# Optimization experiments

Hardware: AMD Instinct MI355X
Metric: run time of the kernel (lower is better)

The kernel has to match this reference:

```python
import jax, jax.numpy as jnp
import numpy as np


def setup_inputs() -> dict:
    key = jax.random.key(0)
    ks = jax.random.split(key, 11)
    B, S, D, H, E, NS = 4, 2048, 1024, 1024, 7, 1
    sc = 0.03125  # ~1/sqrt(D) to keep activations sane
    return {
        "x": jax.random.normal(ks[0], (B, S, D), jnp.float32),
        "gate_w": jax.random.normal(ks[1], (D, E), jnp.float32) * sc,
        "gate_b": jax.random.normal(ks[2], (E,), jnp.float32) * sc,
        "biases": jnp.zeros((E,), jnp.float32),
        "w1": jax.random.normal(ks[3], (E, D, H), jnp.float32) * sc,
        "wg": jax.random.normal(ks[4], (E, D, H), jnp.float32) * sc,
        "w2": jax.random.normal(ks[5], (E, H, D), jnp.float32) * sc,
        "sw1": jax.random.normal(ks[6], (NS, D, H), jnp.float32) * sc,
        "sb1": jax.random.normal(ks[7], (NS, H), jnp.float32) * sc,
        "sw2": jax.random.normal(ks[8], (NS, H, D), jnp.float32) * sc,
        "sb2": jax.random.normal(ks[9], (NS, D), jnp.float32) * sc,
        "top_k": 3,
    }


def reference(x, gate_w, gate_b, biases, w1, wg, w2, sw1, sb1, sw2, sb2, top_k):
    B, S, D = x.shape
    E = w1.shape[0]
    N = B * S
    x2 = x.reshape(N, D)

    # Shared experts: lin1 -> silu -> lin2 (no gate branch), summed over shared dim
    h = jax.nn.silu(jnp.einsum("nd,edh->enh", x2, sw1) + sb1[:, None, :])
    shared = jnp.sum(jnp.einsum("enh,ehd->end", h, sw2) + sb2[:, None, :], axis=0)

    # Router: softmax probs, top-k on bias-adjusted probs, renormalize gathered probs
    probs = jax.nn.softmax(x2 @ gate_w + gate_b, axis=-1)  # [N, E]
    _, topk_idx = jax.lax.top_k(probs + biases, top_k)      # [N, k]
    tp = jnp.take_along_axis(probs, topk_idx, axis=-1)
    tp = tp / jnp.sum(tp, axis=-1, keepdims=True)

    # Combine weights: zero for unselected experts -> [N, E]
    combine = jnp.zeros((N, E), x2.dtype).at[jnp.arange(N)[:, None], topk_idx].add(tp)

    # Routed experts: SwiGLU FFN per expert, weighted combine
    h1 = jax.nn.silu(jnp.einsum("nd,edh->enh", x2, w1)) * jnp.einsum("nd,edh->enh", x2, wg)
    routed = jnp.einsum("enh,ehd,ne->nd", h1, w2, combine)

    return (shared + routed).reshape(B, S, D)
```

## Files before the change

### kernel.cpp

```cpp
#include <hip/hip_runtime.h>
#include <hip/hip_bf16.h>

#define N_TOK 8192
#define DIM   1024
#define NE    7
#define MT_TILES 136

typedef __attribute__((ext_vector_type(8))) short bf16x8;
typedef __attribute__((ext_vector_type(4))) float f32x4;

typedef __attribute__((address_space(3))) ushort lds_us_t;
typedef __attribute__((address_space(1))) const ushort glb_us_t;

__device__ __forceinline__ void gll16(const ushort* g, ushort* l) {
    __builtin_amdgcn_global_load_lds((glb_us_t*)g, (lds_us_t*)l, 16, 0, 0);
}

__device__ __forceinline__ unsigned short f2bf(float f) {
    unsigned int u = __builtin_bit_cast(unsigned int, f);
    u += 0x7fffu + ((u >> 16) & 1u);
    return (unsigned short)(u >> 16);
}

__device__ __forceinline__ float bf2f(unsigned short b) {
    unsigned int u = ((unsigned int)b) << 16;
    return __builtin_bit_cast(float, u);
}

__device__ __forceinline__ float siluf(float v) { return v / (1.f + __expf(-v)); }

__global__ void __launch_bounds__(256)
prep_kernel(const float* __restrict__ w1, const float* __restrict__ wg,
            const float* __restrict__ w2, const float* __restrict__ sw1,
            const float* __restrict__ sw2,
            ushort* __restrict__ w1T, ushort* __restrict__ wgT,
            ushort* __restrict__ w2T,
            const float* __restrict__ x, const float* __restrict__ gw,
            const float* __restrict__ gb, const float* __restrict__ bia,
            int* __restrict__ topk_e, float* __restrict__ topk_w,
            int* __restrict__ counts, ushort* __restrict__ xb)
{
    __shared__ float smem[NE * DIM + 8];
    const int tid = threadIdx.x;
    const int z = blockIdx.z;

    if (z < 23) {
        const float* src; ushort* dst;
        if (z < 7)       { src = w1 + (size_t)z * (DIM*DIM);        dst = w1T + (size_t)z * (DIM*DIM); }
        else if (z < 14) { src = wg + (size_t)(z - 7) * (DIM*DIM);  dst = wgT + (size_t)(z - 7) * (DIM*DIM); }
        else if (z < 21) { src = w2 + (size_t)(z - 14) * (DIM*DIM); dst = w2T + (size_t)(z - 14) * (DIM*DIM); }
        else if (z == 21){ src = sw1; dst = w1T + (size_t)NE * (DIM*DIM); }
        else             { src = sw2; dst = w2T + (size_t)NE * (DIM*DIM); }
        float (*t)[33] = (float(*)[33])smem;
        int bx = blockIdx.x * 32, by = blockIdx.y * 32;
        int lx = tid & 31, ly = tid >> 5;
#pragma unroll
        for (int i = 0; i < 32; i += 8)
            t[ly + i][lx] = src[(size_t)(by + ly + i) * DIM + bx + lx];
        __syncthreads();
#pragma unroll
        for (int i = 0; i < 32; i += 8) {
            int r = ly + i;
            dst[(size_t)(bx + r) * DIM + by + lx] = f2bf(t[lx][r]);
        }
        return;
    }

    float (*gwT)[DIM] = (float(*)[DIM])smem;
    int* cnt = (int*)(smem + NE * DIM);
    const int gblk = blockIdx.y * 32 + blockIdx.x;
    if (tid < NE) cnt[tid] = 0;
    for (int t = tid; t < NE * DIM; t += 256) {
        int d = t / NE, e = t - d * NE;
        gwT[e][d] = gw[t];
    }
    __syncthreads();

    const int lane = tid & 63, wid = tid >> 6;
#pragma unroll
    for (int tt = 0; tt < 2; tt++) {
        const int n = gblk * 8 + wid * 2 + tt;
        const float4* xr = (const float4*)(x + (size_t)n * DIM);
        ushort4* xo = (ushort4*)(xb + (size_t)n * DIM);
        float p[NE];
#pragma unroll
        for (int e = 0; e < NE; e++) p[e] = 0.f;
#pragma unroll
        for (int it = 0; it < 4; it++) {
            int i4 = it * 64 + lane;
            float4 v = xr[i4];
            ushort4 o;
            o.x = f2bf(v.x); o.y = f2bf(v.y); o.z = f2bf(v.z); o.w = f2bf(v.w);
            xo[i4] = o;
            int d = i4 * 4;
#pragma unroll
            for (int e = 0; e < NE; e++) {
                float4 g = *(const float4*)&gwT[e][d];
                p[e] += v.x * g.x + v.y * g.y + v.z * g.z + v.w * g.w;
            }
        }
#pragma unroll
        for (int e = 0; e < NE; e++)
            for (int off = 32; off; off >>= 1) p[e] += __shfl_xor(p[e], off);
        if (lane == 0) {
            float l[NE], m = -1e30f;
#pragma unroll
            for (int e = 0; e < NE; e++) { l[e] = p[e] + gb[e]; m = fmaxf(m, l[e]); }
            float s = 0.f;
#pragma unroll
            for (int e = 0; e < NE; e++) { l[e] = __expf(l[e] - m); s += l[e]; }
            float inv = 1.f / s;
#pragma unroll
            for (int e = 0; e < NE; e++) l[e] *= inv;
            float adj[NE]; bool used[NE];
#pragma unroll
            for (int e = 0; e < NE; e++) { adj[e] = l[e] + bia[e]; used[e] = false; }
            int sel[3]; float w[3]; float ws = 0.f;
            for (int k = 0; k < 3; k++) {
                int b = -1; float bv = -1e30f;
                for (int e = 0; e < NE; e++)
                    if (!used[e] && adj[e] > bv) { bv = adj[e]; b = e; }
                used[b] = true; sel[k] = b; w[k] = l[b]; ws += w[k];
            }
            float iws = 1.f / ws;
            for (int k = 0; k < 3; k++) {
                topk_e[n * 3 + k] = sel[k];
                topk_w[n * 3 + k] = w[k] * iws;
                atomicAdd(&cnt[sel[k]], 1);
            }
        }
    }
    __syncthreads();
    if (tid < NE) atomicAdd(&counts[tid], cnt[tid]);
}

__global__ void __launch_bounds__(64)
setup_kernel(int* __restrict__ ctrl)
{
    __shared__ int eoff[NE + 1];
    __shared__ int tb[NE + 1];
    const int tid = threadIdx.x;
    if (tid == 0) {
        int off = 0, t = 0;
        for (int e = 0; e < NE; e++) {
            eoff[e] = off;
            tb[e] = t;
            ctrl[16 + e] = off;
            int padc = (ctrl[8 + e] + 255) & ~255;
            off += padc;
            t += padc >> 8;
        }
        eoff[NE] = off;  tb[NE] = t;
        ctrl[2] = off;
        ctrl[1] = off + N_TOK;
        ctrl[0] = t + (N_TOK >> 8);
    }
    __syncthreads();
    if (tid <= NE) {
        int* tiles = ctrl + 32;
        int o = eoff[tid];
        int t0 = tb[tid];
        int nt = (tid == NE) ? (N_TOK >> 8) : (tb[tid + 1] - tb[tid]);
        for (int i = 0; i < nt; i++) {
            tiles[(t0 + i) * 2]     = tid;
            tiles[(t0 + i) * 2 + 1] = o + i * 256;
        }
    }
}

__global__ void __launch_bounds__(256)
scatter_kernel(const int* __restrict__ topk_e, int* __restrict__ ctrl,
               int* __restrict__ row_tok, int* __restrict__ slots)
{
    __shared__ int lcnt[NE];
    __shared__ int base[NE];
    const int tid = threadIdx.x;
    const int n = blockIdx.x * 256 + tid;
    if (tid < NE) lcnt[tid] = 0;
    __syncthreads();
    row_tok[ctrl[2] + n] = n;
    int e[3], ofs[3];
#pragma unroll
    for (int k = 0; k < 3; k++) {
        e[k] = topk_e[n * 3 + k];
        ofs[k] = atomicAdd(&lcnt[e[k]], 1);
    }
    __syncthreads();
    if (tid < NE) base[tid] = atomicAdd(&ctrl[16 + tid], lcnt[tid]);
    __syncthreads();
#pragma unroll
    for (int k = 0; k < 3; k++) {
        int slot = base[e[k]] + ofs[k];
        row_tok[slot] = n;
        slots[n * 3 + k] = slot;
    }
}


__global__ void __launch_bounds__(512, 2)
g1_kernel(const ushort* __restrict__ Xb, const ushort* __restrict__ W1,
          const ushort* __restrict__ WG, const float* __restrict__ sb1,
          ushort* __restrict__ H, const int* __restrict__ row_tok,
          const int* __restrict__ ctrl)
{
    __shared__ ushort lds[32768];
    int bx, col0;
    {
        int L = blockIdx.x + blockIdx.y * MT_TILES;
        int D = (L & 7) * MT_TILES + (L >> 3);
        bx = D >> 3;  col0 = (D & 7) * 128;
    }
    if (bx >= ctrl[0]) return;
    const int e     = ctrl[32 + 2*bx];
    const int slot0 = ctrl[32 + 2*bx + 1];
    const bool gated = (e != NE);
    const int tt = threadIdx.x;
    const int lane = tt & 63, wid = tt >> 6;
    const int wm = wid >> 1, wn = wid & 1;
    const int wofs = wid * 512;

    const int slog = (tt & 7) ^ ((tt >> 3) & 7);
    const int kk0 = (slog & 3) * 8;
    const int r0 = ((tt >> 3) << 1) + (slog >> 2);
    const ushort* pA0 = Xb + (size_t)row_tok[slot0 + r0] * DIM + kk0;
    const ushort* pA1 = Xb + (size_t)row_tok[slot0 + r0 + 128] * DIM + kk0;
    const ushort* B1e = W1 + (size_t)e * (DIM*DIM);
    const ushort* B2e = gated ? (WG + (size_t)e * (DIM*DIM))
                              : (W1 + (size_t)NE * (DIM*DIM));
    const ushort* pB1 = B1e + (size_t)(col0 + r0) * DIM + kk0;
    const ushort* pB2 = B2e + (size_t)(col0 + r0) * DIM + kk0;

    const int hi = lane >> 4, lr = lane & 15;
    int aoff[4], boff[4];
#pragma unroll
    for (int m = 0; m < 4; m++) {
        int row = wm*64 + m*16 + lr;
        int lrow = row >> 1;
        int sl = ((row & 1) << 2) | hi;
        aoff[m] = lrow*64 + (sl ^ (lrow & 7))*8;
    }
#pragma unroll
    for (int n = 0; n < 4; n++) {
        int oc = wn*64 + n*16 + lr;
        int lrow = oc >> 1;
        int sl = ((oc & 1) << 2) | hi;
        boff[n] = lrow*64 + (sl ^ (lrow & 7))*8;
    }

    f32x4 zero4 = {0.f, 0.f, 0.f, 0.f};
    f32x4 acc1[4][4], acc2[4][4];
#pragma unroll
    for (int m = 0; m < 4; m++)
#pragma unroll
        for (int n = 0; n < 4; n++) { acc1[m][n] = zero4; acc2[m][n] = zero4; }

    auto stage = [&](int buf, int kte) {
        ushort* b = &lds[buf * 16384];
        gll16(pA0 + kte, b + wofs);
        gll16(pA1 + kte, b + 4096 + wofs);
        gll16(pB1 + kte, b + 8192 + wofs);
        if (gated) gll16(pB2 + kte, b + 12288 + wofs);
    };
    auto compute = [&](int buf) {
        const ushort* Ab = &lds[buf * 16384];
        const ushort* Bb = Ab + 8192;
        bf16x8 a[4], bv[4];
#pragma unroll
        for (int m = 0; m < 4; m++) a[m] = *(const bf16x8*)(Ab + aoff[m]);
#pragma unroll
        for (int n = 0; n < 4; n++) bv[n] = *(const bf16x8*)(Bb + boff[n]);
        __builtin_amdgcn_s_setprio(1);
#pragma unroll
        for (int m = 0; m < 4; m++)
#pragma unroll
            for (int n = 0; n < 4; n++)
                acc1[m][n] = __builtin_amdgcn_mfma_f32_16x16x32_bf16(a[m], bv[n], acc1[m][n], 0, 0, 0);
        __builtin_amdgcn_s_setprio(0);
        if (gated) {
            const ushort* B2b = Ab + 12288;
            bf16x8 b2[4];
#pragma unroll
            for (int n = 0; n < 4; n++) b2[n] = *(const bf16x8*)(B2b + boff[n]);
            __builtin_amdgcn_s_setprio(1);
#pragma unroll
            for (int m = 0; m < 4; m++)
#pragma unroll
                for (int n = 0; n < 4; n++)
                    acc2[m][n] = __builtin_amdgcn_mfma_f32_16x16x32_bf16(a[m], b2[n], acc2[m][n], 0, 0, 0);
            __builtin_amdgcn_s_setprio(0);
        }
    };

    stage(0, 0);
    asm volatile("s_waitcnt vmcnt(0)" ::: "memory");
    __builtin_amdgcn_s_barrier();
    asm volatile("" ::: "memory");
    for (int t = 0; t < 31; ++t) {
        stage((t + 1) & 1, (t + 1) * 32);
        compute(t & 1);
        asm volatile("s_waitcnt vmcnt(0)" ::: "memory");
        __builtin_amdgcn_s_barrier();
        asm volatile("" ::: "memory");
    }
    compute(1);

#pragma unroll
    for (int m = 0; m < 4; m++)
#pragma unroll
        for (int n = 0; n < 4; n++)
#pragma unroll
            for (int r = 0; r < 4; r++) {
                int row = slot0 + wm*64 + m*16 + hi*4 + r;
                int col = col0 + wn*64 + n*16 + lr;
                float v1 = acc1[m][n][r];
                float h = gated ? siluf(v1) * acc2[m][n][r]
                                : siluf(v1 + sb1[col]);
                H[(size_t)row * DIM + col] = f2bf(h);
            }
}

__global__ void __launch_bounds__(512, 2)
g2_kernel(const ushort* __restrict__ H, const ushort* __restrict__ W2,
          const float* __restrict__ sb2, float* __restrict__ out,
          ushort* __restrict__ y2, const int* __restrict__ ctrl)
{
    __shared__ ushort lds[24576];
    int bx, col0;
    {
        int L = blockIdx.x + blockIdx.y * MT_TILES;
        int D = (L & 7) * MT_TILES + (L >> 3);
        bx = D >> 3;  col0 = (D & 7) * 128;
    }
    if (bx >= ctrl[0]) return;
    const int e     = ctrl[32 + 2*bx];
    const int slot0 = ctrl[32 + 2*bx + 1];
    const int sbase = ctrl[2];
    const int tt = threadIdx.x;
    const int lane = tt & 63, wid = tt >> 6;
    const int wm = wid >> 1, wn = wid & 1;
    const int wofs = wid * 512;

    const int slog = (tt & 7) ^ ((tt >> 3) & 7);
    const int kk0 = (slog & 3) * 8;
    const int r0 = ((tt >> 3) << 1) + (slog >> 2);
    const ushort* pA0 = H + (size_t)(slot0 + r0) * DIM + kk0;
    const ushort* pA1 = H + (size_t)(slot0 + r0 + 128) * DIM + kk0;
    const ushort* Be  = W2 + (size_t)e * (DIM*DIM);
    const ushort* pB1 = Be + (size_t)(col0 + r0) * DIM + kk0;

    const int hi = lane >> 4, lr = lane & 15;
    int aoff[4], boff[4];
#pragma unroll
    for (int m = 0; m < 4; m++) {
        int row = wm*64 + m*16 + lr;
        int lrow = row >> 1;
        int sl = ((row & 1) << 2) | hi;
        aoff[m] = lrow*64 + (sl ^ (lrow & 7))*8;
    }
#pragma unroll
    for (int n = 0; n < 4; n++) {
        int oc = wn*64 + n*16 + lr;
        int lrow = oc >> 1;
        int sl = ((oc & 1) << 2) | hi;
        boff[n] = lrow*64 + (sl ^ (lrow & 7))*8;
    }

    f32x4 zero4 = {0.f, 0.f, 0.f, 0.f};
    f32x4 acc[4][4];
#pragma unroll
    for (int m = 0; m < 4; m++)
#pragma unroll
        for (int n = 0; n < 4; n++) acc[m][n] = zero4;

    auto stage = [&](int buf, int kte) {
        ushort* b = &lds[buf * 12288];
        gll16(pA0 + kte, b + wofs);
        gll16(pA1 + kte, b + 4096 + wofs);
        gll16(pB1 + kte, b + 8192 + wofs);
    };
    auto compute = [&](int buf) {
        const ushort* Ab = &lds[buf * 12288];
        const ushort* Bb = Ab + 8192;
        bf16x8 a[4], bv[4];
#pragma unroll
        for (int m = 0; m < 4; m++) a[m] = *(const bf16x8*)(Ab + aoff[m]);
#pragma unroll
        for (int n = 0; n < 4; n++) bv[n] = *(const bf16x8*)(Bb + boff[n]);
        __builtin_amdgcn_s_setprio(1);
#pragma unroll
        for (int m = 0; m < 4; m++)
#pragma unroll
            for (int n = 0; n < 4; n++)
                acc[m][n] = __builtin_amdgcn_mfma_f32_16x16x32_bf16(a[m], bv[n], acc[m][n], 0, 0, 0);
        __builtin_amdgcn_s_setprio(0);
    };

    stage(0, 0);
    asm volatile("s_waitcnt vmcnt(0)" ::: "memory");
    __builtin_amdgcn_s_barrier();
    asm volatile("" ::: "memory");
    for (int t = 0; t < 31; ++t) {
        stage((t + 1) & 1, (t + 1) * 32);
        compute(t & 1);
        asm volatile("s_waitcnt vmcnt(0)" ::: "memory");
        __builtin_amdgcn_s_barrier();
        asm volatile("" ::: "memory");
    }
    compute(1);

#pragma unroll
    for (int m = 0; m < 4; m++)
#pragma unroll
        for (int n = 0; n < 4; n++)
#pragma unroll
            for (int r = 0; r < 4; r++) {
                int row = slot0 + wm*64 + m*16 + hi*4 + r;
                int col = col0 + wn*64 + n*16 + lr;
                float v = acc[m][n][r];
                if (e != NE) y2[(size_t)row * DIM + col] = f2bf(v);
                else         out[(size_t)(row - sbase) * DIM + col] = v + sb2[col];
            }
}

__global__ void __launch_bounds__(256)
combine_kernel(const ushort* __restrict__ y2, const int* __restrict__ slots,
               const float* __restrict__ topk_w, float* __restrict__ out)
{
    __shared__ int ss[3];
    __shared__ float sw[3];
    const int n = blockIdx.x, tid = threadIdx.x;
    if (tid < 3) { ss[tid] = slots[n * 3 + tid]; sw[tid] = topk_w[n * 3 + tid]; }
    __syncthreads();
    float4* o4 = (float4*)(out + (size_t)n * DIM);
    float4 o = o4[tid];
#pragma unroll
    for (int k = 0; k < 3; k++) {
        const ushort4 yv = *(const ushort4*)(y2 + (size_t)ss[k] * DIM + tid * 4);
        float w = sw[k];
        o.x += w * bf2f(yv.x);
        o.y += w * bf2f(yv.y);
        o.z += w * bf2f(yv.z);
        o.w += w * bf2f(yv.w);
    }
    o4[tid] = o;
}

extern "C" void kernel_launch(void* const* d_in, const int* in_sizes, int n_in,
                              void* d_out, int out_size, void* d_ws, size_t ws_size,
                              hipStream_t stream)
{
    const float* x    = (const float*)d_in[0];
    const float* gw   = (const float*)d_in[1];
    const float* gb   = (const float*)d_in[2];
    const float* bia  = (const float*)d_in[3];
    const float* w1   = (const float*)d_in[4];
    const float* wg   = (const float*)d_in[5];
    const float* w2   = (const float*)d_in[6];
    const float* sw1  = (const float*)d_in[7];
    const float* sb1  = (const float*)d_in[8];
    const float* sw2  = (const float*)d_in[9];
    const float* sb2  = (const float*)d_in[10];
    float* out = (float*)d_out;

    char* ws = (char*)d_ws;
    int*    ctrl   = (int*)   (ws + 0);
    int*    topk_e = (int*)   (ws + 4096);
    float*  topk_w = (float*) (ws + 102400);
    int*    slots  = (int*)   (ws + 200704);
    int*    row_tok= (int*)   (ws + 299008);
    ushort* w1T    = (ushort*)(ws + 437248);
    ushort* wgT    = (ushort*)(ws + 17214464);
    ushort* w2T    = (ushort*)(ws + 31894528);
    ushort* h1     = (ushort*)(ws + 48671744);
    ushort* y2     = (ushort*)(ws + 119450624);
    ushort* xb     = y2;

    hipMemsetAsync(ctrl, 0, 4096, stream);
    hipMemsetAsync(row_tok, 0, 34560 * 4, stream);
    prep_kernel<<<dim3(32, 32, 24), 256, 0, stream>>>(w1, wg, w2, sw1, sw2,
                                                      w1T, wgT, w2T,
                                                      x, gw, gb, bia,
                                                      topk_e, topk_w, ctrl + 8, xb);
    setup_kernel<<<1, 64, 0, stream>>>(ctrl);
    scatter_kernel<<<N_TOK / 256, 256, 0, stream>>>(topk_e, ctrl, row_tok, slots);

    g1_kernel<<<dim3(MT_TILES, 8), 512, 0, stream>>>(xb, w1T, wgT, sb1, h1,
                                                     row_tok, ctrl);
    g2_kernel<<<dim3(MT_TILES, 8), 512, 0, stream>>>(h1, w2T, sb2, out, y2, ctrl);
    combine_kernel<<<N_TOK, 256, 0, stream>>>(y2, slots, topk_w, out);
}
```

Baseline: 360.1 us.

## Load weight B fragments directly from global into registers, skipping LDS

In both grouped GEMM kernels, B (weight) tiles are no longer staged through LDS. Each wave now loads its own B fragments straight from global memory into registers, double-buffered across k-steps, and LDS holds only the gathered A tiles. This shrinks LDS use and removes the LDS write/read round trip for B. The cost is that the two wm-waves sharing a column slice each fetch the same B data from global, raising global and L2 traffic, and it adds register pressure under launch_bounds(512,2).

Result: slower. 720.1 us (+100.0%).

```diff
diff --git a/kernel.cpp b/kernel.cpp
--- a/kernel.cpp
+++ b/kernel.cpp
@@ -203,7 +203,7 @@
           ushort* __restrict__ H, const int* __restrict__ row_tok,
           const int* __restrict__ ctrl)
 {
-    __shared__ ushort lds[32768];
+    __shared__ ushort lds[16384];
     int bx, col0;
     {
         int L = blockIdx.x + blockIdx.y * MT_TILES;
@@ -218,20 +218,21 @@
     const int lane = tt & 63, wid = tt >> 6;
     const int wm = wid >> 1, wn = wid & 1;
     const int wofs = wid * 512;
+    const int hi = lane >> 4, lr = lane & 15;
 
     const int slog = (tt & 7) ^ ((tt >> 3) & 7);
     const int kk0 = (slog & 3) * 8;
     const int r0 = ((tt >> 3) << 1) + (slog >> 2);
     const ushort* pA0 = Xb + (size_t)row_tok[slot0 + r0] * DIM + kk0;
     const ushort* pA1 = Xb + (size_t)row_tok[slot0 + r0 + 128] * DIM + kk0;
+
     const ushort* B1e = W1 + (size_t)e * (DIM*DIM);
     const ushort* B2e = gated ? (WG + (size_t)e * (DIM*DIM))
                               : (W1 + (size_t)NE * (DIM*DIM));
-    const ushort* pB1 = B1e + (size_t)(col0 + r0) * DIM + kk0;
-    const ushort* pB2 = B2e + (size_t)(col0 + r0) * DIM + kk0;
-
-    const int hi = lane >> 4, lr = lane & 15;
-    int aoff[4], boff[4];
+    const ushort* pBg1 = B1e + (size_t)(col0 + wn*64 + lr) * DIM + hi*8;
+    const ushort* pBg2 = B2e + (size_t)(col0 + wn*64 + lr) * DIM + hi*8;
+
+    int aoff[4];
 #pragma unroll
     for (int m = 0; m < 4; m++) {
         int row = wm*64 + m*16 + lr;
@@ -239,13 +240,6 @@
         int sl = ((row & 1) << 2) | hi;
         aoff[m] = lrow*64 + (sl ^ (lrow & 7))*8;
     }
-#pragma unroll
-    for (int n = 0; n < 4; n++) {
-        int oc = wn*64 + n*16 + lr;
-        int lrow = oc >> 1;
-        int sl = ((oc & 1) << 2) | hi;
-        boff[n] = lrow*64 + (sl ^ (lrow & 7))*8;
-    }
 
     f32x4 zero4 = {0.f, 0.f, 0.f, 0.f};
     f32x4 acc1[4][4], acc2[4][4];
@@ -254,33 +248,33 @@
 #pragma unroll
         for (int n = 0; n < 4; n++) { acc1[m][n] = zero4; acc2[m][n] = zero4; }
 
-    auto stage = [&](int buf, int kte) {
-        ushort* b = &lds[buf * 16384];
+    bf16x8 bc1[4], bc2[4], bn1[4], bn2[4];
+
+    auto stageA = [&](int buf, int kte) {
+        ushort* b = &lds[buf * 8192];
         gll16(pA0 + kte, b + wofs);
         gll16(pA1 + kte, b + 4096 + wofs);
-        gll16(pB1 + kte, b + 8192 + wofs);
-        if (gated) gll16(pB2 + kte, b + 12288 + wofs);
     };
-    auto compute = [&](int buf) {
-        const ushort* Ab = &lds[buf * 16384];
-        const ushort* Bb = Ab + 8192;
-        bf16x8 a[4], bv[4];
+    auto loadB = [&](bf16x8* d1, bf16x8* d2, int kt) {
+#pragma unroll
+        for (int n = 0; n < 4; n++) {
+            d1[n] = *(const bf16x8*)(pBg1 + (size_t)n * 16 * DIM + kt * 32);
+            if (gated) d2[n] = *(const bf16x8*)(pBg2 + (size_t)n * 16 * DIM + kt * 32);
+        }
+    };
+    auto compute = [&](int buf, const bf16x8* b1, const bf16x8* b2) {
+        const ushort* Ab = &lds[buf * 8192];
+        bf16x8 a[4];
 #pragma unroll
         for (int m = 0; m < 4; m++) a[m] = *(const bf16x8*)(Ab + aoff[m]);
-#pragma unroll
-        for (int n = 0; n < 4; n++) bv[n] = *(const bf16x8*)(Bb + boff[n]);
         __builtin_amdgcn_s_setprio(1);
 #pragma unroll
         for (int m = 0; m < 4; m++)
 #pragma unroll
             for (int n = 0; n < 4; n++)
-                acc1[m][n] = __builtin_amdgcn_mfma_f32_16x16x32_bf16(a[m], bv[n], acc1[m][n], 0, 0, 0);
+                acc1[m][n] = __builtin_amdgcn_mfma_f32_16x16x32_bf16(a[m], b1[n], acc1[m][n], 0, 0, 0);
         __builtin_amdgcn_s_setprio(0);
         if (gated) {
-            const ushort* B2b = Ab + 12288;
-            bf16x8 b2[4];
-#pragma unroll
-            for (int n = 0; n < 4; n++) b2[n] = *(const bf16x8*)(B2b + boff[n]);
             __builtin_amdgcn_s_setprio(1);
 #pragma unroll
             for (int m = 0; m < 4; m++)
@@ -291,18 +285,29 @@
         }
     };
 
-    stage(0, 0);
+    stageA(0, 0); loadB(bc1, bc2, 0);
     asm volatile("s_waitcnt vmcnt(0)" ::: "memory");
     __builtin_amdgcn_s_barrier();
     asm volatile("" ::: "memory");
-    for (int t = 0; t < 31; ++t) {
-        stage((t + 1) & 1, (t + 1) * 32);
-        compute(t & 1);
+    for (int tp = 0; tp < 15; ++tp) {
+        int t = tp * 2;
+        stageA(1, (t + 1) * 32); loadB(bn1, bn2, t + 1);
+        compute(0, bc1, bc2);
         asm volatile("s_waitcnt vmcnt(0)" ::: "memory");
         __builtin_amdgcn_s_barrier();
         asm volatile("" ::: "memory");
-    }
-    compute(1);
+        stageA(0, (t + 2) * 32); loadB(bc1, bc2, t + 2);
+        compute(1, bn1, bn2);
+        asm volatile("s_waitcnt vmcnt(0)" ::: "memory");
+        __builtin_amdgcn_s_barrier();
+        asm volatile("" ::: "memory");
+    }
+    stageA(1, 31 * 32); loadB(bn1, bn2, 31);
+    compute(0, bc1, bc2);
+    asm volatile("s_waitcnt vmcnt(0)" ::: "memory");
+    __builtin_amdgcn_s_barrier();
+    asm volatile("" ::: "memory");
+    compute(1, bn1, bn2);
 
 #pragma unroll
     for (int m = 0; m < 4; m++)
@@ -324,7 +329,7 @@
           const float* __restrict__ sb2, float* __restrict__ out,
           ushort* __restrict__ y2, const int* __restrict__ ctrl)
 {
-    __shared__ ushort lds[24576];
+    __shared__ ushort lds[16384];
     int bx, col0;
     {
         int L = blockIdx.x + blockIdx.y * MT_TILES;
@@ -339,6 +344,7 @@
     const int lane = tt & 63, wid = tt >> 6;
     const int wm = wid >> 1, wn = wid & 1;
     const int wofs = wid * 512;
+    const int hi = lane >> 4, lr = lane & 15;
 
     const int slog = (tt & 7) ^ ((tt >> 3) & 7);
     const int kk0 = (slog & 3) * 8;
@@ -346,10 +352,9 @@
     const ushort* pA0 = H + (size_t)(slot0 + r0) * DIM + kk0;
     const ushort* pA1 = H + (size_t)(slot0 + r0 + 128) * DIM + kk0;
     const ushort* Be  = W2 + (size_t)e * (DIM*DIM);
-    const ushort* pB1 = Be + (size_t)(col0 + r0) * DIM + kk0;
-
-    const int hi = lane >> 4, lr = lane & 15;
-    int aoff[4], boff[4];
+    const ushort* pBg = Be + (size_t)(col0 + wn*64 + lr) * DIM + hi*8;
+
+    int aoff[4];
 #pragma unroll
     for (int m = 0; m < 4; m++) {
         int row = wm*64 + m*16 + lr;
@@ -357,13 +362,6 @@
         int sl = ((row & 1) << 2) | hi;
         aoff[m] = lrow*64 + (sl ^ (lrow & 7))*8;
     }
-#pragma unroll
-    for (int n = 0; n < 4; n++) {
-        int oc = wn*64 + n*16 + lr;
-        int lrow = oc >> 1;
-        int sl = ((oc & 1) << 2) | hi;
-        boff[n] = lrow*64 + (sl ^ (lrow & 7))*8;
-    }
 
     f32x4 zero4 = {0.f, 0.f, 0.f, 0.f};
     f32x4 acc[4][4];
@@ -372,41 +370,55 @@
 #pragma unroll
         for (int n = 0; n < 4; n++) acc[m][n] = zero4;
 
-    auto stage = [&](int buf, int kte) {
-        ushort* b = &lds[buf * 12288];
+    bf16x8 bc[4], bn[4];
+
+    auto stageA = [&](int buf, int kte) {
+        ushort* b = &lds[buf * 8192];
         gll16(pA0 + kte, b + wofs);
         gll16(pA1 + kte, b + 4096 + wofs);
-        gll16(pB1 + kte, b + 8192 + wofs);
     };
-    auto compute = [&](int buf) {
-        const ushort* Ab = &lds[buf * 12288];
-        const ushort* Bb = Ab + 8192;
-        bf16x8 a[4], bv[4];
+    auto loadB = [&](bf16x8* d, int kt) {
+#pragma unroll
+        for (int n = 0; n < 4; n++)
+            d[n] = *(const bf16x8*)(pBg + (size_t)n * 16 * DIM + kt * 32);
+    };
+    auto compute = [&](int buf, const bf16x8* b) {
+        const ushort* Ab = &lds[buf * 8192];
+        bf16x8 a[4];
 #pragma unroll
         for (int m = 0; m < 4; m++) a[m] = *(const bf16x8*)(Ab + aoff[m]);
-#pragma unroll
-        for (int n = 0; n < 4; n++) bv[n] = *(const bf16x8*)(Bb + boff[n]);
         __builtin_amdgcn_s_setprio(1);
 #pragma unroll
         for (int m = 0; m < 4; m++)
 #pragma unroll
             for (int n = 0; n < 4; n++)
-                acc[m][n] = __builtin_amdgcn_mfma_f32_16x16x32_bf16(a[m], bv[n], acc[m][n], 0, 0, 0);
+                acc[m][n] = __builtin_amdgcn_mfma_f32_16x16x32_bf16(a[m], b[n], acc[m][n], 0, 0, 0);
         __builtin_amdgcn_s_setprio(0);
     };
 
-    stage(0, 0);
+    stageA(0, 0); loadB(bc, 0);
     asm volatile("s_waitcnt vmcnt(0)" ::: "memory");
     __builtin_amdgcn_s_barrier();
     asm volatile("" ::: "memory");
-    for (int t = 0; t < 31; ++t) {
-        stage((t + 1) & 1, (t + 1) * 32);
-        compute(t & 1);
+    for (int tp = 0; tp < 15; ++tp) {
+        int t = tp * 2;
+        stageA(1, (t + 1) * 32); loadB(bn, t + 1);
+        compute(0, bc);
         asm volatile("s_waitcnt vmcnt(0)" ::: "memory");
         __builtin_amdgcn_s_barrier();
         asm volatile("" ::: "memory");
-    }
-    compute(1);
+        stageA(0, (t + 2) * 32); loadB(bc, t + 2);
+        compute(1, bn);
+        asm volatile("s_waitcnt vmcnt(0)" ::: "memory");
+        __builtin_amdgcn_s_barrier();
+        asm volatile("" ::: "memory");
+    }
+    stageA(1, 31 * 32); loadB(bn, 31);
+    compute(0, bc);
+    asm volatile("s_waitcnt vmcnt(0)" ::: "memory");
+    __builtin_amdgcn_s_barrier();
+    asm volatile("" ::: "memory");
+    compute(1, bn);
 
 #pragma unroll
     for (int m = 0; m < 4; m++)
```
